# Optimization experiments

Measured on AMD Instinct MI355X. Metric: run time of the kernel, lower is better.

## Reference

```python
import jax, jax.numpy as jnp
import numpy as np

B, L, HID, LOW = 1024, 64, 512, 20
TEMP = 1.0
EPS = 1e-20


def setup_inputs() -> dict:
    key = jax.random.key(0)
    ks = jax.random.split(key, 8)
    input_h = jax.random.normal(ks[0], (B, L, HID), jnp.float32)
    input_c = jax.random.normal(ks[1], (B, L, HID), jnp.float32)
    length = jax.random.randint(ks[2], (B,), L // 2, L + 1)          # valid lengths in [L/2, L]
    u_noise = jax.random.uniform(ks[3], (L - 1, B, L - 1), jnp.float32)  # gumbel uniforms per level
    s = 1.0 / np.sqrt(HID)
    W_reduce = jax.random.uniform(ks[4], (HID, LOW), jnp.float32, -s, s)
    b_reduce = jnp.zeros((LOW,), jnp.float32)
    s2 = 1.0 / np.sqrt(2 * LOW)
    W_comp = jax.random.uniform(ks[5], (2 * LOW, 5 * LOW), jnp.float32, -s2, s2)
    b_comp = jnp.zeros((5 * LOW,), jnp.float32)
    query = jax.random.normal(ks[6], (LOW,), jnp.float32) / np.sqrt(LOW)
    return dict(input_h=input_h, input_c=input_c, W_reduce=W_reduce, b_reduce=b_reduce,
                W_comp=W_comp, b_comp=b_comp, query=query, u_noise=u_noise, length=length)


def _treelstm(hl, cl, hr, cr, W, b):
    # BinaryTreeLSTMLayer.forward: concat children, one Linear to 5 gates
    v = jnp.concatenate([hl, hr], axis=-1) @ W + b          # (B, n, 5*LOW)
    i_, fl, fr, u_, o = jnp.split(v, 5, axis=-1)
    c = cl * jax.nn.sigmoid(fl + 1.0) + cr * jax.nn.sigmoid(fr + 1.0) \
        + jnp.tanh(u_) * jax.nn.sigmoid(i_)
    h = jax.nn.sigmoid(o) * jnp.tanh(c)
    return h, c


def _masked_softmax(logits, mask):
    probs = jax.nn.softmax(logits, axis=1)
    probs = probs * mask + EPS
    return probs / probs.sum(axis=1, keepdims=True)


def _st_gumbel(logits, u, mask):
    g = -jnp.log(-jnp.log(u + EPS) + EPS)                   # gumbel noise (non-diff, matches .data)
    y = _masked_softmax((logits + g) / TEMP, mask)
    y_hard = jax.nn.one_hot(jnp.argmax(y, axis=1), y.shape[1], dtype=y.dtype)
    return jax.lax.stop_gradient(y_hard - y) + y            # straight-through


def _forward(input_h, input_c, W_reduce, b_reduce, W_comp, b_comp, query, u_noise, length):
    h = input_h @ W_reduce + b_reduce                       # (B, L, LOW)  reduce_dim
    c = input_c @ W_reduce + b_reduce
    length_mask = (jnp.arange(L)[None, :] < length[:, None]).astype(h.dtype)  # (B, L)
    for i in range(L - 1):                                  # sequential DP over pyramid levels
        hl, cl = h[:, :-1], c[:, :-1]
        hr, cr = h[:, 1:], c[:, 1:]
        nh, nc = _treelstm(hl, cl, hr, cr, W_comp, b_comp)  # (B, L-1-i, LOW) all adjacent merges
        if i < L - 2:
            logits = nh @ query                             # dot_nd scoring, (B, L-1-i)
            sel = _st_gumbel(logits, u_noise[i, :, :L - 1 - i], length_mask[:, i + 1:])
            cum = jnp.cumsum(sel, axis=1)
            left = (1.0 - cum)[..., None]                   # keep old left spans
            right = (cum - sel)[..., None]                  # shift old right spans
            se = sel[..., None]
            nh = se * nh + left * hl + right * hr
            nc = se * nc + left * cl + right * cr
        done = length_mask[:, i + 1][:, None, None]         # update_state done_mask
        h = done * nh + (1.0 - done) * hl
        c = done * nc + (1.0 - done) * cl
    return h[:, 0]                                          # (B, LOW) root hidden state


def reference(input_h, input_c, W_reduce, b_reduce, W_comp, b_comp, query, u_noise, length):
    return _forward(input_h, input_c, W_reduce, b_reduce, W_comp, b_comp, query, u_noise, length)
```

## Files before the change

kernel.cpp:

```cpp
#include <hip/hip_runtime.h>
#include <cmath>
#include <cfloat>

namespace {

constexpr int kB   = 1024;
constexpr int kL   = 64;
constexpr int kHid = 512;
constexpr int kLow = 20;
constexpr int kLM1 = 63;
constexpr int kRowElems = kL * kLow;

typedef float v2f __attribute__((ext_vector_type(2)));

__device__ __forceinline__ float fsig(float x) {
  return __builtin_amdgcn_rcpf(1.0f + __expf(-x));
}
__device__ __forceinline__ float ftanhf(float x) {
  return 1.0f - 2.0f * __builtin_amdgcn_rcpf(1.0f + __expf(2.0f * x));
}
__device__ __forceinline__ int rdl_i(int v, int l) {
  return __builtin_amdgcn_readlane(v, l);
}
__device__ __forceinline__ float rdl_f(float v, int l) {
  return __int_as_float(__builtin_amdgcn_readlane(__float_as_int(v), l));
}

#define DPPI(v, ctrl) __builtin_amdgcn_update_dpp((v), (v), (ctrl), 0xF, 0xF, false)
#define DPPF(v, ctrl) __int_as_float(DPPI(__float_as_int(v), (ctrl)))
#define DPPF0(v, ctrl)                                                        \
  __int_as_float(__builtin_amdgcn_update_dpp(0, __float_as_int(v), (ctrl),    \
                                             0xF, 0xF, true))
#define UMAX_STAGE(CTRL)                                                      \
  {                                                                           \
    const unsigned o_ = (unsigned)DPPI((int)m, CTRL);                         \
    m = (m > o_) ? m : o_;                                                    \
  }

#define PKFMA(ACC, X, W)                                                      \
  asm("v_pk_fma_f32 %0, %1, %2, %0" : "+v"(ACC) : "v"(X), "v"(W))

#define LOGIT_REDUCE(PR_)                                                     \
  {                                                                           \
    PR_ += DPPF0(PR_, 0xB1);                                                  \
    PR_ += DPPF0(PR_, 0x4E);                                                  \
    PR_ += DPPF0(PR_, 0x141);                                                 \
    PR_ += DPPF0(PR_, 0x140);                                                 \
    PR_ += DPPF0(PR_, 0x142);                                                 \
  }

__global__ __launch_bounds__(256, 6)
void reduce_kernel(const float* __restrict__ Xh, const float* __restrict__ Xc,
                   const float* __restrict__ W, const float* __restrict__ bv,
                   float* __restrict__ H0, float* __restrict__ C0) {
  __shared__ float xs[5184];
  __shared__ float wsm[64 * 20];

  const int bid = blockIdx.x;
  const float* __restrict__ X = (bid < kB) ? Xh : Xc;
  float* __restrict__ O       = (bid < kB) ? H0 : C0;
  const int b = bid & (kB - 1);
  X += (size_t)b * kL * kHid;
  O += (size_t)b * kRowElems;

  const int tid  = threadIdx.x;
  const int wave = tid >> 6;
  const int lane = tid & 63;

  float acc[20];
#pragma unroll
  for (int d = 0; d < 20; ++d) acc[d] = 0.0f;

  for (int ch = 0; ch < 8; ++ch) {
    __syncthreads();
#pragma unroll
    for (int r = 0; r < 4; ++r) {
      int f   = r * 256 + tid;
      int row = f >> 4;
      int c4  = (f & 15) << 2;
      float4 v = *(const float4*)(X + row * kHid + ch * 64 + c4);
      *(float4*)(xs + row * 65 + c4) = v;
    }
#pragma unroll
    for (int r = 0; r < 5; ++r) {
      int f = r * 256 + tid;
      wsm[f] = W[ch * 1280 + f];
    }
    __syncthreads();
#pragma unroll
    for (int kk = 0; kk < 16; ++kk) {
      int k = wave * 16 + kk;
      float x = xs[lane * 65 + k];
      const float4* wp = (const float4*)(wsm + k * 20);
      float4 w0 = wp[0], w1 = wp[1], w2 = wp[2], w3 = wp[3], w4 = wp[4];
      acc[0]  = fmaf(x, w0.x, acc[0]);  acc[1]  = fmaf(x, w0.y, acc[1]);
      acc[2]  = fmaf(x, w0.z, acc[2]);  acc[3]  = fmaf(x, w0.w, acc[3]);
      acc[4]  = fmaf(x, w1.x, acc[4]);  acc[5]  = fmaf(x, w1.y, acc[5]);
      acc[6]  = fmaf(x, w1.z, acc[6]);  acc[7]  = fmaf(x, w1.w, acc[7]);
      acc[8]  = fmaf(x, w2.x, acc[8]);  acc[9]  = fmaf(x, w2.y, acc[9]);
      acc[10] = fmaf(x, w2.z, acc[10]); acc[11] = fmaf(x, w2.w, acc[11]);
      acc[12] = fmaf(x, w3.x, acc[12]); acc[13] = fmaf(x, w3.y, acc[13]);
      acc[14] = fmaf(x, w3.z, acc[14]); acc[15] = fmaf(x, w3.w, acc[15]);
      acc[16] = fmaf(x, w4.x, acc[16]); acc[17] = fmaf(x, w4.y, acc[17]);
      acc[18] = fmaf(x, w4.z, acc[18]); acc[19] = fmaf(x, w4.w, acc[19]);
    }
  }

  __syncthreads();
  float* red = xs;
#pragma unroll
  for (int d = 0; d < 20; ++d) red[wave * 1280 + lane * 20 + d] = acc[d];
  __syncthreads();
#pragma unroll
  for (int r = 0; r < 5; ++r) {
    int f = r * 256 + tid;
    float s = (red[f] + red[1280 + f]) + (red[2560 + f] + red[3840 + f]);
    O[f] = s + bv[f % 20];
  }
}

#define EVAL_UNIT(A_, B2_, PS_, DD_, HN_)                                     \
  {                                                                           \
    float ai = bcs[DD_], af = bcs[20 + DD_], ag = bcs[40 + DD_],              \
          au = bcs[60 + DD_], ao = bcs[80 + DD_];                             \
    const int xa_ = (A_)*20, xb_ = (B2_)*20, wr_ = (DD_)*44;                  \
    _Pragma("unroll")                                                         \
    for (int kq = 0; kq < 10; ++kq) {                                         \
      const float4 xq = (kq < 5)                                              \
          ? *(const float4*)(h_state + xa_ + kq * 4)                          \
          : *(const float4*)(h_state + xb_ + (kq - 5) * 4);                   \
      const float4 wi = *(const float4*)(Wt + wr_ + kq * 4);                  \
      const float4 wf = *(const float4*)(Wt + 880  + wr_ + kq * 4);           \
      const float4 wg = *(const float4*)(Wt + 1760 + wr_ + kq * 4);           \
      const float4 wu = *(const float4*)(Wt + 2640 + wr_ + kq * 4);           \
      const float4 wo = *(const float4*)(Wt + 3520 + wr_ + kq * 4);           \
      ai = fmaf(xq.x, wi.x, ai); ai = fmaf(xq.y, wi.y, ai);                   \
      ai = fmaf(xq.z, wi.z, ai); ai = fmaf(xq.w, wi.w, ai);                   \
      af = fmaf(xq.x, wf.x, af); af = fmaf(xq.y, wf.y, af);                   \
      af = fmaf(xq.z, wf.z, af); af = fmaf(xq.w, wf.w, af);                   \
      ag = fmaf(xq.x, wg.x, ag); ag = fmaf(xq.y, wg.y, ag);                   \
      ag = fmaf(xq.z, wg.z, ag); ag = fmaf(xq.w, wg.w, ag);                   \
      au = fmaf(xq.x, wu.x, au); au = fmaf(xq.y, wu.y, au);                   \
      au = fmaf(xq.z, wu.z, au); au = fmaf(xq.w, wu.w, au);                   \
      ao = fmaf(xq.x, wo.x, ao); ao = fmaf(xq.y, wo.y, ao);                   \
      ao = fmaf(xq.z, wo.z, ao); ao = fmaf(xq.w, wo.w, ao);                   \
    }                                                                         \
    const float cl_ = c_state[(A_)*20 + (DD_)],                               \
                cr_ = c_state[(B2_)*20 + (DD_)];                              \
    const float cn_ = cl_ * fsig(af + 1.0f) + cr_ * fsig(ag + 1.0f) +         \
                      ftanhf(au) * fsig(ai);                                  \
    (HN_) = fsig(ao) * ftanhf(cn_);                                           \
    nh[(PS_)*20 + (DD_)] = (HN_);                                             \
    nc[(PS_)*20 + (DD_)] = cn_;                                               \
  }

__global__ __launch_bounds__(64, 1)
void pyramid_kernel(const float* __restrict__ H0, const float* __restrict__ C0,
                    const float* __restrict__ Wc, const float* __restrict__ bcg,
                    const float* __restrict__ query, const float* __restrict__ U,
                    const int* __restrict__ length, float* __restrict__ out) {
  __shared__ float h_state[64 * 20];
  __shared__ float c_state[64 * 20];
  __shared__ float nh[63 * 20];
  __shared__ float nc[63 * 20];
  __shared__ float Wt[100 * 44];
  __shared__ float bcs[100];
  __shared__ float qvs[20];
  __shared__ float sc[200];

  const int b    = blockIdx.x;
  const int lane = threadIdx.x;
  const int p    = lane >> 5;
  const int dd   = lane & 31;
  const int ddc  = dd < 20 ? dd : 19;
  int len = length[b];
  len = len < 1 ? 1 : (len > 64 ? 64 : len);

  {
    const float4* h4 = (const float4*)(H0 + (size_t)b * kRowElems);
    const float4* c4 = (const float4*)(C0 + (size_t)b * kRowElems);
#pragma unroll
    for (int r = 0; r < 5; ++r) {
      int f = r * 64 + lane;
      ((float4*)h_state)[f] = h4[f];
      ((float4*)c_state)[f] = c4[f];
    }
  }
  for (int f = lane; f < 4000; f += 64) {
    int c = f / 40, k = f - c * 40;
    Wt[c * 44 + k] = Wc[k * 100 + c];
  }
  for (int f = lane; f < 100; f += 64) bcs[f] = bcg[f];
  if (lane < 20) qvs[lane] = query[lane];

  const bool cact = lane < 50;
  const int  c0   = cact ? 2 * lane : 0;
  const int  c1   = c0 + 1;
  v2f Wv0[20], Wv1[20];
#pragma unroll
  for (int k2 = 0; k2 < 20; ++k2) {
    Wv0[k2] = (v2f){Wc[(2 * k2) * 100 + c0], Wc[(2 * k2 + 1) * 100 + c0]};
    Wv1[k2] = (v2f){Wc[(2 * k2) * 100 + c1], Wc[(2 * k2 + 1) * 100 + c1]};
  }
  const float bb0 = bcg[c0], bb1 = bcg[c1];
  const float qv_r = query[ddc];

  int   idx_r  = lane;
  int   pidx_r = lane;
  float lgt_r  = -FLT_MAX;

  const int col = lane < 62 ? lane : 62;
  const float u_row0 = U[b * kLM1 + col];
  float u_c = (kLM1 > 1) ? U[1 * (kB * kLM1) + b * kLM1 + col] : 0.0f;

#pragma unroll 1
  for (int r = 0; r < 20; ++r) {
    int uu = r * 64 + lane;
    if (uu < 1260) {
      int pp = uu / 20, d2 = uu - pp * 20;
      float hn_;
      EVAL_UNIT(pp, pp + 1, pp, d2, hn_);
      (void)hn_;
    }
  }
  if (lane < 63) {
    float s = 0.0f;
#pragma unroll
    for (int q = 0; q < 5; ++q) {
      const float4 t  = *(const float4*)(nh  + lane * 20 + q * 4);
      const float4 qv = *(const float4*)(qvs + q * 4);
      s = fmaf(t.x, qv.x, s); s = fmaf(t.y, qv.y, s);
      s = fmaf(t.z, qv.z, s); s = fmaf(t.w, qv.w, s);
    }
    lgt_r = s;
  }

  float gcur = -__logf(-__logf(u_row0 + 1e-20f) + 1e-20f);

  const int nIter = len - 1;
#pragma unroll 1
  for (int i = 0; i < nIter; ++i) {
    const int n = kL - i;

    const float zf = lgt_r + gcur;
    const unsigned ub = __float_as_uint(zf);
    unsigned key = ((int)ub < 0) ? ~ub : (ub | 0x80000000u);
    const bool valid = (lane <= n - 2) && ((i + 1 + lane) < len);
    if (!valid) key = 0u;
    unsigned m = key;
    UMAX_STAGE(0xB1);
    UMAX_STAGE(0x4E);
    UMAX_STAGE(0x141);
    UMAX_STAGE(0x140);
    UMAX_STAGE(0x142);
    UMAX_STAGE(0x143);
    const unsigned gmax = (unsigned)rdl_i((int)m, 63);
    const unsigned long long bal = __ballot(valid && (key == gmax));
    const int k = (int)(__ffsll(bal) - 1);

    float u_d = 0.0f;
    if (i + 2 <= kLM1 - 1) u_d = U[(i + 2) * (kB * kLM1) + b * kLM1 + col];

    const int km1 = (k >= 1) ? k - 1 : 0;
    const int kp2 = (k <= n - 3) ? k + 2 : 0;
    const int tgt = rdl_i(idx_r,  k);
    const int psk = rdl_i(pidx_r, k);
    const int iA  = rdl_i(idx_r,  km1);
    const int pA  = rdl_i(pidx_r, km1);
    const int iB  = rdl_i(idx_r,  kp2);

    v2f hA2[10], hT2[10], hB2[10];
#pragma unroll
    for (int q = 0; q < 5; ++q) {
      const float4 tA = *(const float4*)(h_state + iA * 20 + q * 4);
      const float4 tT = *(const float4*)(nh + psk * 20 + q * 4);
      const float4 tB = *(const float4*)(h_state + iB * 20 + q * 4);
      hA2[2*q]   = (v2f){tA.x, tA.y};  hA2[2*q+1] = (v2f){tA.z, tA.w};
      hT2[2*q]   = (v2f){tT.x, tT.y};  hT2[2*q+1] = (v2f){tT.z, tT.w};
      hB2[2*q]   = (v2f){tB.x, tB.y};  hB2[2*q+1] = (v2f){tB.z, tB.w};
    }
    const float cA_ = c_state[iA * 20 + ddc];
    const float cT_ = nc[psk * 20 + ddc];
    const float cB_ = c_state[iB * 20 + ddc];

    if (lane < 20) {
      h_state[tgt * 20 + lane] = nh[psk * 20 + lane];
      c_state[tgt * 20 + lane] = nc[psk * 20 + lane];
    }

    {
      int   sI = DPPI(idx_r,  0x101);
      int   sP = DPPI(pidx_r, 0x101);
      float sL = DPPF(lgt_r,  0x101);
      const int   bi16 = rdl_i(idx_r, 16),  bi32 = rdl_i(idx_r, 32),
                  bi48 = rdl_i(idx_r, 48);
      const int   bp16 = rdl_i(pidx_r, 16), bp32 = rdl_i(pidx_r, 32),
                  bp48 = rdl_i(pidx_r, 48);
      const float bl16 = rdl_f(lgt_r, 16),  bl32 = rdl_f(lgt_r, 32),
                  bl48 = rdl_f(lgt_r, 48);
      if (lane == 15) { sI = bi16; sP = bp16; sL = bl16; }
      if (lane == 31) { sI = bi32; sP = bp32; sL = bl32; }
      if (lane == 47) { sI = bi48; sP = bp48; sL = bl48; }
      const bool doI = (lane >= k + 1) && (lane <= n - 2);
      const bool doP = (lane >= k + 1) && (lane <= n - 3);
      if (doI) idx_r = sI;
      if (doP) { pidx_r = sP; lgt_r = sL; }
    }

    if (i < len - 2) {
      const bool hasA = (k >= 1);
      const bool hasB = (k <= n - 3);

      v2f aA0 = (v2f){0.f, 0.f}, aA1 = aA0, aB0 = aA0, aB1 = aA0;
#pragma unroll
      for (int k2 = 0; k2 < 10; ++k2) {
        PKFMA(aA0, hA2[k2], Wv0[k2]);
        PKFMA(aA1, hA2[k2], Wv1[k2]);
        PKFMA(aB0, hT2[k2], Wv0[k2]);
        PKFMA(aB1, hT2[k2], Wv1[k2]);
      }
#pragma unroll
      for (int k2 = 10; k2 < 20; ++k2) {
        PKFMA(aA0, hT2[k2 - 10], Wv0[k2]);
        PKFMA(aA1, hT2[k2 - 10], Wv1[k2]);
        PKFMA(aB0, hB2[k2 - 10], Wv0[k2]);
        PKFMA(aB1, hB2[k2 - 10], Wv1[k2]);
      }

      if (cact) {
        *(v2f*)(sc + c0)       = (v2f){aA0[0] + aA0[1] + bb0,
                                       aA1[0] + aA1[1] + bb1};
        *(v2f*)(sc + 100 + c0) = (v2f){aB0[0] + aB0[1] + bb0,
                                       aB1[0] + aB1[1] + bb1};
      }

      const float* scp = sc + p * 100;
      const float i_ = scp[ddc],      fl_ = scp[20 + ddc],
                  fr_ = scp[40 + ddc], u_ = scp[60 + ddc],
                  o_ = scp[80 + ddc];
      const float cl_ = (p == 0) ? cA_ : cT_;
      const float cr_ = (p == 0) ? cT_ : cB_;
      const float cn_ = cl_ * fsig(fl_ + 1.0f) + cr_ * fsig(fr_ + 1.0f) +
                        ftanhf(u_) * fsig(i_);
      const float hn_ = fsig(o_) * ftanhf(cn_);
      const int   slot = (p == 0) ? pA : psk;
      const bool  mine = (p == 0) ? hasA : hasB;
      if (mine && dd < 20) {
        nh[slot * 20 + dd] = hn_;
        nc[slot * 20 + dd] = cn_;
      }
      float pr = (dd < 20) ? hn_ * qv_r : 0.0f;
      LOGIT_REDUCE(pr);
      const float vA = rdl_f(pr, 31);
      const float vB = rdl_f(pr, 63);
      if (hasA && lane == k - 1) lgt_r = vA;
      if (hasB && lane == k)     lgt_r = vB;
    }

    gcur = -__logf(-__logf(u_c + 1e-20f) + 1e-20f);
    u_c  = u_d;
  }

  const int root = rdl_i(idx_r, 0);
  if (lane < 20) {
    out[b * 20 + lane] = h_state[root * 20 + lane];
  }
}

}

extern "C" void kernel_launch(void* const* d_in, const int* in_sizes, int n_in,
                              void* d_out, int out_size, void* d_ws, size_t ws_size,
                              hipStream_t stream) {
  const float* input_h  = (const float*)d_in[0];
  const float* input_c  = (const float*)d_in[1];
  const float* W_reduce = (const float*)d_in[2];
  const float* b_reduce = (const float*)d_in[3];
  const float* W_comp   = (const float*)d_in[4];
  const float* b_comp   = (const float*)d_in[5];
  const float* query    = (const float*)d_in[6];
  const float* u_noise  = (const float*)d_in[7];
  const int*   length   = (const int*)d_in[8];
  float* out = (float*)d_out;

  float* H0 = (float*)d_ws;
  float* C0 = H0 + (size_t)kB * kL * kLow;

  reduce_kernel<<<dim3(2 * kB), dim3(256), 0, stream>>>(
      input_h, input_c, W_reduce, b_reduce, H0, C0);
  pyramid_kernel<<<dim3(kB), dim3(64), 0, stream>>>(
      H0, C0, W_comp, b_comp, query, u_noise, length, out);
}
```

Before: 158.9 us.

## Precompute next level's argmax over unchanged logits before the TreeLSTM merge

Moves the per-level gumbel argmax off the critical path. The wave-wide max reduction for the next level now runs over the logits that do not change (all but the two slots next to the merge) before the TreeLSTM compute. After the compute, the two fresh logits are combined with that partial max using scalar compares. This shortens the serial dependency chain from the new logits to the next selection, at the cost of extra readlanes and more complex tie-breaking logic.

```diff
diff --git a/kernel.cpp b/kernel.cpp
--- a/kernel.cpp
+++ b/kernel.cpp
@@ -24,6 +24,10 @@
 }
 __device__ __forceinline__ float rdl_f(float v, int l) {
   return __int_as_float(__builtin_amdgcn_readlane(__float_as_int(v), l));
+}
+__device__ __forceinline__ unsigned sortkey(float z) {
+  const unsigned ub = __float_as_uint(z);
+  return ((int)ub < 0) ? ~ub : (ub | 0x80000000u);
 }
 
 #define DPPI(v, ctrl) __builtin_amdgcn_update_dpp((v), (v), (ctrl), 0xF, 0xF, false)
@@ -211,7 +215,7 @@
 
   const int col = lane < 62 ? lane : 62;
   const float u_row0 = U[b * kLM1 + col];
-  float u_c = (kLM1 > 1) ? U[1 * (kB * kLM1) + b * kLM1 + col] : 0.0f;
+  float u_c = U[(size_t)1 * (kB * kLM1) + b * kLM1 + col];
 
 #pragma unroll 1
   for (int r = 0; r < 20; ++r) {
@@ -235,31 +239,30 @@
     lgt_r = s;
   }
 
-  float gcur = -__logf(-__logf(u_row0 + 1e-20f) + 1e-20f);
+  int kCur = 0;
+  {
+    const float g0 = -__logf(-__logf(u_row0 + 1e-20f) + 1e-20f);
+    unsigned key = sortkey(lgt_r + g0);
+    const bool valid = (lane <= 62) && ((1 + lane) < len);
+    if (!valid) key = 0u;
+    unsigned m = key;
+    UMAX_STAGE(0xB1); UMAX_STAGE(0x4E); UMAX_STAGE(0x141);
+    UMAX_STAGE(0x140); UMAX_STAGE(0x142); UMAX_STAGE(0x143);
+    const unsigned gmax = (unsigned)rdl_i((int)m, 63);
+    const unsigned long long bal = __ballot(valid && (key == gmax));
+    kCur = bal ? (int)(__ffsll(bal) - 1) : 0;
+  }
 
   const int nIter = len - 1;
 #pragma unroll 1
   for (int i = 0; i < nIter; ++i) {
     const int n = kL - i;
-
-    const float zf = lgt_r + gcur;
-    const unsigned ub = __float_as_uint(zf);
-    unsigned key = ((int)ub < 0) ? ~ub : (ub | 0x80000000u);
-    const bool valid = (lane <= n - 2) && ((i + 1 + lane) < len);
-    if (!valid) key = 0u;
-    unsigned m = key;
-    UMAX_STAGE(0xB1);
-    UMAX_STAGE(0x4E);
-    UMAX_STAGE(0x141);
-    UMAX_STAGE(0x140);
-    UMAX_STAGE(0x142);
-    UMAX_STAGE(0x143);
-    const unsigned gmax = (unsigned)rdl_i((int)m, 63);
-    const unsigned long long bal = __ballot(valid && (key == gmax));
-    const int k = (int)(__ffsll(bal) - 1);
+    const int k = kCur;
+
+    const float gnx = -__logf(-__logf(u_c + 1e-20f) + 1e-20f);
 
     float u_d = 0.0f;
-    if (i + 2 <= kLM1 - 1) u_d = U[(i + 2) * (kB * kLM1) + b * kLM1 + col];
+    if (i + 2 <= kLM1 - 1) u_d = U[(size_t)(i + 2) * (kB * kLM1) + b * kLM1 + col];
 
     const int km1 = (k >= 1) ? k - 1 : 0;
     const int kp2 = (k <= n - 3) ? k + 2 : 0;
@@ -305,6 +308,24 @@
       const bool doP = (lane >= k + 1) && (lane <= n - 3);
       if (doI) idx_r = sI;
       if (doP) { pidx_r = sP; lgt_r = sL; }
+    }
+
+    unsigned keyM;
+    int jM;
+    bool hasM;
+    {
+      const int n2 = n - 1;
+      unsigned key = sortkey(lgt_r + gnx);
+      const bool validM = (lane <= n2 - 2) && ((i + 2 + lane) < len) &&
+                          (lane != k - 1) && (lane != k);
+      if (!validM) key = 0u;
+      unsigned m = key;
+      UMAX_STAGE(0xB1); UMAX_STAGE(0x4E); UMAX_STAGE(0x141);
+      UMAX_STAGE(0x140); UMAX_STAGE(0x142); UMAX_STAGE(0x143);
+      keyM = (unsigned)rdl_i((int)m, 63);
+      const unsigned long long bal = __ballot(validM && (key == keyM));
+      hasM = bal != 0;
+      jM   = hasM ? (int)(__ffsll(bal) - 1) : 64;
     }
 
     if (i < len - 2) {
@@ -355,10 +376,21 @@
       const float vB = rdl_f(pr, 63);
       if (hasA && lane == k - 1) lgt_r = vA;
       if (hasB && lane == k)     lgt_r = vB;
-    }
-
-    gcur = -__logf(-__logf(u_c + 1e-20f) + 1e-20f);
-    u_c  = u_d;
+
+      const int n2 = n - 1;
+      const bool vA_ok = hasA && ((i + 2 + (k - 1)) < len);
+      const bool vB_ok = hasB && (k <= n2 - 2) && ((i + 2 + k) < len);
+      const unsigned keyA = sortkey(vA + rdl_f(gnx, km1));
+      const unsigned keyB = sortkey(vB + rdl_f(gnx, k));
+      unsigned bk = 0u;
+      int bj = 64;
+      if (vA_ok) { bk = keyA; bj = k - 1; }
+      if (vB_ok && (keyB > bk || (keyB == bk && k < bj))) { bk = keyB; bj = k; }
+      if (hasM  && (keyM > bk || (keyM == bk && jM < bj))) { bk = keyM; bj = jM; }
+      kCur = (bj < 64) ? bj : 0;
+    }
+
+    u_c = u_d;
   }
 
   const int root = rdl_i(idx_r, 0);
```

After: 175.3 us. 1.1x slower.
